# Kernel tuning notes

Measured on AMD Instinct MI355X. Metric: run time of the kernel, lower is better.

## Reference

```python
import jax, jax.numpy as jnp
import numpy as np

ROPE_BASE = 10000.0

def _rope_cos_sin(T, d, dtype):
    inv_freq = 1.0 / (ROPE_BASE ** (jnp.arange(0, d, 2, dtype=jnp.float32) / d))
    t = jnp.arange(T, dtype=jnp.float32)
    freqs = t[:, None] * inv_freq[None, :]           # [T, d/2]
    emb = jnp.concatenate([freqs, freqs], axis=-1)   # [T, d]
    return jnp.cos(emb).astype(dtype), jnp.sin(emb).astype(dtype)

def _rotate_half(x):
    x1, x2 = jnp.split(x, 2, axis=-1)
    return jnp.concatenate([-x2, x1], axis=-1)

def setup_inputs() -> dict:
    key = jax.random.key(0)
    k1, k2, k3, k4 = jax.random.split(key, 4)
    B, T, C, H = 4, 4096, 1024, 64
    x = jax.random.normal(k1, (B, T, C), dtype=jnp.float32)
    s = 1.0 / np.sqrt(C)
    Wq = jax.random.normal(k2, (H, C), dtype=jnp.float32) * s
    Wk = jax.random.normal(k3, (H, C), dtype=jnp.float32) * s
    Wv = jax.random.normal(k4, (H, C), dtype=jnp.float32) * s
    return {"x": x, "Wq": Wq, "Wk": Wk, "Wv": Wv}

def reference(x, Wq, Wk, Wv):
    B, T, C = x.shape
    H = Wq.shape[0]
    q = jnp.einsum('btc,hc->bth', x, Wq)
    k = jnp.einsum('btc,hc->bth', x, Wk)
    v = jnp.einsum('btc,hc->bth', x, Wv)
    cos, sin = _rope_cos_sin(T, H, x.dtype)
    q = q * cos + _rotate_half(q) * sin
    k = k * cos + _rotate_half(k) * sin
    # NOTE: original scales by dim_model**-0.5 (C), not head_size
    wei = jnp.einsum('bth,bsh->bts', q, k) * (C ** -0.5)
    causal = jnp.tril(jnp.ones((T, T), dtype=bool))
    wei = jnp.where(causal, wei, -jnp.inf)
    wei = jax.nn.softmax(wei, axis=-1)
    # dropout p=0.0 (identity)
    out = jnp.einsum('bts,bsh->bth', wei, v)
    return out
```

## Files before the change

kernel.cpp:

```cpp
#include <hip/hip_runtime.h>
#include <hip/hip_bf16.h>
#include <math.h>

typedef __attribute__((ext_vector_type(8))) __bf16 bf16x8;
typedef __attribute__((ext_vector_type(4))) float f32x4;
typedef __attribute__((ext_vector_type(16))) float f32x16;
typedef __attribute__((ext_vector_type(4))) float float4_t;
typedef __attribute__((ext_vector_type(4))) unsigned int uint4_t;

#define NB 4
#define TSEQ 4096
#define CD 1024
#define HD 64
#define NCH 8
#define CHT 8

static __device__ __forceinline__ unsigned short f2bf(float f) {
    union { float f; unsigned u; } v; v.f = f;
    unsigned r = v.u + 0x7fffu + ((v.u >> 16) & 1u);
    return (unsigned short)(r >> 16);
}
static __device__ __forceinline__ unsigned int pack2bf(float lo, float hi) {
    return (unsigned int)f2bf(lo) | ((unsigned int)f2bf(hi) << 16);
}

__global__ __launch_bounds__(256) void wcvt_kernel(const float* __restrict__ wq,
                                                   const float* __restrict__ wk,
                                                   const float* __restrict__ wv,
                                                   unsigned short* __restrict__ wb) {
    int i = blockIdx.x * 256 + threadIdx.x;
    int j = i >> 10;
    int col = i & 1023;
    int jb = j >> 4, off = j & 15;
    int sub = ((jb & 1) << 5) | ((jb & 2) << 3);
    int srcrow = (jb < 8) ? (sub + off) : ((jb - 8) * 16 + off);
    const float* src = (jb < 4) ? wq : ((jb < 8) ? wk : wv);
    wb[i] = f2bf(src[srcrow * 1024 + col]);
}

__global__ __launch_bounds__(256) void qkv_kernel(const float* __restrict__ x,
                                                  const unsigned short* __restrict__ wb,
                                                  unsigned short* __restrict__ qo,
                                                  unsigned short* __restrict__ ko,
                                                  unsigned short* __restrict__ vt) {
    __shared__ unsigned short xs[64][72];
    __shared__ unsigned short ws[64][72];
    const int tid = threadIdx.x;
    const int wave = tid >> 6, lane = tid & 63;
    const int lr = lane & 15;
    const int lk = (lane >> 4) << 3;
    const int rowg = (lane >> 4) << 2;
    const int row0 = blockIdx.x * 64;
    const int cb = blockIdx.y * 64;

    f32x4 acc[4];
#pragma unroll
    for (int i = 0; i < 4; ++i) acc[i] = (f32x4){0.f, 0.f, 0.f, 0.f};

    const int sr = tid >> 2;
    const int sc = (tid & 3) << 4;

    for (int k0 = 0; k0 < CD; k0 += 64) {
        __syncthreads();
        {
            const float4_t* s4 =
                reinterpret_cast<const float4_t*>(x + (size_t)(row0 + sr) * CD + k0 + sc);
            alignas(16) unsigned short tmp[16];
#pragma unroll
            for (int j = 0; j < 4; ++j) {
                float4_t f = s4[j];
#pragma unroll
                for (int e = 0; e < 4; ++e) tmp[j * 4 + e] = f2bf(f[e]);
            }
            *reinterpret_cast<uint4_t*>(&xs[sr][sc]) = *reinterpret_cast<const uint4_t*>(&tmp[0]);
            *reinterpret_cast<uint4_t*>(&xs[sr][sc + 8]) = *reinterpret_cast<const uint4_t*>(&tmp[8]);
        }
        {
            const uint4_t* wsrc =
                reinterpret_cast<const uint4_t*>(wb + (size_t)(cb + sr) * CD + k0 + sc);
            *reinterpret_cast<uint4_t*>(&ws[sr][sc]) = wsrc[0];
            *reinterpret_cast<uint4_t*>(&ws[sr][sc + 8]) = wsrc[1];
        }
        __syncthreads();
#pragma unroll
        for (int kk = 0; kk < 2; ++kk) {
            bf16x8 a = *reinterpret_cast<const bf16x8*>(&xs[wave * 16 + lr][kk * 32 + lk]);
#pragma unroll
            for (int c = 0; c < 4; ++c) {
                bf16x8 bfr = *reinterpret_cast<const bf16x8*>(&ws[c * 16 + lr][kk * 32 + lk]);
                acc[c] = __builtin_amdgcn_mfma_f32_16x16x32_bf16(a, bfr, acc[c], 0, 0, 0);
            }
        }
    }

    const int gr0 = row0 + wave * 16 + rowg;
    const int bidx = gr0 >> 12;
    const int tb = gr0 & (TSEQ - 1);
    if (blockIdx.y < 2) {
        unsigned short* o = (blockIdx.y == 0) ? qo : ko;
        const float sc2 = (blockIdx.y == 0) ? 0.045084218764560315f : 1.0f;
        const float l2b = 0.4152410118609215f;
        const float invf0 = exp2f(-(float)lr * l2b);
        const float invf1 = exp2f(-(float)(lr + 16) * l2b);
#pragma unroll
        for (int r = 0; r < 4; ++r) {
            float t = (float)(tb + r);
            float s0, c0, s1, c1;
            sincosf(t * invf0, &s0, &c0);
            sincosf(t * invf1, &s1, &c1);
            size_t ro = (size_t)(gr0 + r) * HD;
            float lo, hi;
            lo = acc[0][r]; hi = acc[1][r];
            o[ro + 0 + lr]  = f2bf((lo * c0 - hi * s0) * sc2);
            o[ro + 32 + lr] = f2bf((hi * c0 + lo * s0) * sc2);
            lo = acc[2][r]; hi = acc[3][r];
            o[ro + 16 + lr] = f2bf((lo * c1 - hi * s1) * sc2);
            o[ro + 48 + lr] = f2bf((hi * c1 + lo * s1) * sc2);
        }
    } else {
#pragma unroll
        for (int r = 0; r < 4; ++r) {
            size_t vbase = (size_t)bidx * HD * TSEQ + (size_t)(tb + r);
            vt[vbase + (size_t)(0 + lr) * TSEQ]  = f2bf(acc[0][r]);
            vt[vbase + (size_t)(16 + lr) * TSEQ] = f2bf(acc[1][r]);
            vt[vbase + (size_t)(32 + lr) * TSEQ] = f2bf(acc[2][r]);
            vt[vbase + (size_t)(48 + lr) * TSEQ] = f2bf(acc[3][r]);
        }
    }
}

__global__ __launch_bounds__(128, 3) void attn_partial(const unsigned short* __restrict__ q,
                                                       const unsigned short* __restrict__ k,
                                                       const unsigned short* __restrict__ vt,
                                                       float* __restrict__ po,
                                                       float* __restrict__ pm,
                                                       float* __restrict__ pl) {
    const int chunk = blockIdx.x, qt = blockIdx.y, b = blockIdx.z;
    const int kt0 = chunk * CHT;
    if (kt0 > qt) return;
    const int ktend = min(qt, kt0 + CHT - 1);

    __shared__ unsigned short ks[64][72];
    __shared__ unsigned short vs[64][72];
    const int tid = threadIdx.x;
    const int wave = tid >> 6, lane = tid & 63;
    const int l31 = lane & 31;
    const int h = lane >> 5;
    const int h8 = h << 3;
    const int qrow0 = qt * 64 + wave * 32;
    const int qpos = qrow0 + l31;

    const unsigned short* qb_ = q + ((size_t)(b * TSEQ + qpos)) * HD + h8;
    bf16x8 qf[4];
#pragma unroll
    for (int s = 0; s < 4; ++s)
        qf[s] = *reinterpret_cast<const bf16x8*>(qb_ + 16 * s);

    f32x16 oacc[2];
#pragma unroll
    for (int dt = 0; dt < 2; ++dt)
#pragma unroll
        for (int r = 0; r < 16; ++r) oacc[dt][r] = 0.f;
    float mreg = -INFINITY;
    float lsum = 0.f;

    const int srow = tid >> 1;
    const int scol = (tid & 1) << 5;
    const unsigned short* kbase = k + (size_t)b * TSEQ * HD;
    const unsigned short* vbase = vt + (size_t)b * HD * TSEQ;
    uint4_t kr[4], vr[4];
    {
        const int s0l = kt0 * 64;
        const unsigned short* kp = kbase + (size_t)(s0l + srow) * HD + scol;
        const unsigned short* vp = vbase + (size_t)srow * TSEQ + s0l + scol;
#pragma unroll
        for (int j = 0; j < 4; ++j) {
            kr[j] = *reinterpret_cast<const uint4_t*>(kp + 8 * j);
            vr[j] = *reinterpret_cast<const uint4_t*>(vp + 8 * j);
        }
    }

    for (int kt = kt0; kt <= ktend; ++kt) {
        const int s0 = kt * 64;
        __syncthreads();
#pragma unroll
        for (int j = 0; j < 4; ++j) {
            *reinterpret_cast<uint4_t*>(&ks[srow][scol + 8 * j]) = kr[j];
            *reinterpret_cast<uint4_t*>(&vs[srow][scol + 8 * j]) = vr[j];
        }
        __syncthreads();
        if (kt < ktend) {
            const int s0l = s0 + 64;
            const unsigned short* kp = kbase + (size_t)(s0l + srow) * HD + scol;
            const unsigned short* vp = vbase + (size_t)srow * TSEQ + s0l + scol;
#pragma unroll
            for (int j = 0; j < 4; ++j) {
                kr[j] = *reinterpret_cast<const uint4_t*>(kp + 8 * j);
                vr[j] = *reinterpret_cast<const uint4_t*>(vp + 8 * j);
            }
        }

        f32x16 sacc[2];
#pragma unroll
        for (int blk = 0; blk < 2; ++blk)
#pragma unroll
            for (int r = 0; r < 16; ++r) sacc[blk][r] = 0.f;
#pragma unroll
        for (int s = 0; s < 4; ++s) {
            bf16x8 ka = *reinterpret_cast<const bf16x8*>(&ks[l31][16 * s + h8]);
            bf16x8 kb2 = *reinterpret_cast<const bf16x8*>(&ks[32 + l31][16 * s + h8]);
            sacc[0] = __builtin_amdgcn_mfma_f32_32x32x16_bf16(ka, qf[s], sacc[0], 0, 0, 0);
            sacc[1] = __builtin_amdgcn_mfma_f32_32x32x16_bf16(kb2, qf[s], sacc[1], 0, 0, 0);
        }

        if (kt == qt) {
#pragma unroll
            for (int blk = 0; blk < 2; ++blk)
#pragma unroll
                for (int r = 0; r < 16; ++r) {
                    int kvpos = s0 + 32 * blk + (r & 3) + ((r >> 2) << 3) + (h << 2);
                    if (kvpos > qpos) sacc[blk][r] = -INFINITY;
                }
        }

        float mx = -INFINITY;
#pragma unroll
        for (int blk = 0; blk < 2; ++blk)
#pragma unroll
            for (int r = 0; r < 16; ++r) mx = fmaxf(mx, sacc[blk][r]);
        mx = fmaxf(mx, __shfl_xor(mx, 32, 64));
        float mnew = fmaxf(mreg, mx);
        float corr = __builtin_amdgcn_exp2f(mreg - mnew);
        mreg = mnew;
        float psum = 0.f;
        float pvv[2][16];
#pragma unroll
        for (int blk = 0; blk < 2; ++blk)
#pragma unroll
            for (int r = 0; r < 16; ++r) {
                float p = __builtin_amdgcn_exp2f(sacc[blk][r] - mnew);
                pvv[blk][r] = p;
                psum += p;
            }
        psum += __shfl_xor(psum, 32, 64);
        lsum = lsum * corr + psum;
#pragma unroll
        for (int dt = 0; dt < 2; ++dt)
#pragma unroll
            for (int r = 0; r < 16; ++r) oacc[dt][r] *= corr;

        unsigned int cw[2][4][2];
#pragma unroll
        for (int blk = 0; blk < 2; ++blk)
#pragma unroll
            for (int G = 0; G < 4; ++G) {
                cw[blk][G][0] = pack2bf(pvv[blk][4 * G], pvv[blk][4 * G + 1]);
                cw[blk][G][1] = pack2bf(pvv[blk][4 * G + 2], pvv[blk][4 * G + 3]);
            }

        const bool hif = (h == 1);
#pragma unroll
        for (int s = 0; s < 4; ++s) {
            const int blk = s >> 1, base = (s & 1) << 1;
            unsigned int a0 = cw[blk][base][0],     a1 = cw[blk][base][1];
            unsigned int b0 = cw[blk][base + 1][0], b1 = cw[blk][base + 1][1];
            unsigned int s0w = hif ? a0 : b0;
            unsigned int s1w = hif ? a1 : b1;
            unsigned int r0 = __shfl_xor(s0w, 32, 64);
            unsigned int r1 = __shfl_xor(s1w, 32, 64);
            uint4_t pw;
            pw[0] = hif ? r0 : a0;
            pw[1] = hif ? r1 : a1;
            pw[2] = hif ? b0 : r0;
            pw[3] = hif ? b1 : r1;
            bf16x8 pfrag = *reinterpret_cast<const bf16x8*>(&pw);
            bf16x8 v0 = *reinterpret_cast<const bf16x8*>(&vs[l31][16 * s + h8]);
            bf16x8 v1 = *reinterpret_cast<const bf16x8*>(&vs[32 + l31][16 * s + h8]);
            oacc[0] = __builtin_amdgcn_mfma_f32_32x32x16_bf16(v0, pfrag, oacc[0], 0, 0, 0);
            oacc[1] = __builtin_amdgcn_mfma_f32_32x32x16_bf16(v1, pfrag, oacc[1], 0, 0, 0);
        }
    }

    const int slot = (((b << 6) + qt) << 3) + chunk;
    float* pob = po + (size_t)slot * 4096;
#pragma unroll
    for (int dt = 0; dt < 2; ++dt)
#pragma unroll
        for (int r = 0; r < 16; ++r) {
            int d = 32 * dt + (r & 3) + ((r >> 2) << 3) + (h << 2);
            pob[d * 64 + wave * 32 + l31] = oacc[dt][r];
        }
    if (h == 0) {
        pm[slot * 64 + wave * 32 + l31] = mreg;
        pl[slot * 64 + wave * 32 + l31] = lsum;
    }
}

__global__ __launch_bounds__(256) void attn_combine(const float* __restrict__ po,
                                                    const float* __restrict__ pm,
                                                    const float* __restrict__ pl,
                                                    float* __restrict__ out) {
    __shared__ float sm[64][68];
    const int bq = blockIdx.x;
    const int qt = bq & 63;
    const int nch = (qt >> 3) + 1;
    const int qi = threadIdx.x & 63;
    const int dg = threadIdx.x >> 6;
    const int sbase = bq << 3;

    float M = -INFINITY;
    for (int c = 0; c < nch; ++c) M = fmaxf(M, pm[(sbase + c) * 64 + qi]);
    float L = 0.f;
    float acc[16];
#pragma unroll
    for (int j = 0; j < 16; ++j) acc[j] = 0.f;
    for (int c = 0; c < nch; ++c) {
        int s = sbase + c;
        float w = exp2f(pm[s * 64 + qi] - M);
        L += w * pl[s * 64 + qi];
        const float* p = po + (size_t)s * 4096 + qi;
#pragma unroll
        for (int j = 0; j < 16; ++j) acc[j] += w * p[(dg * 16 + j) * 64];
    }
    float inv = 1.f / L;
#pragma unroll
    for (int j = 0; j < 16; ++j) sm[qi][dg * 16 + j] = acc[j] * inv;
    __syncthreads();
    const int row = threadIdx.x >> 2;
    const int cg = (threadIdx.x & 3) << 4;
    float4_t* dst = reinterpret_cast<float4_t*>(out + (size_t)bq * 4096 + row * 64 + cg);
#pragma unroll
    for (int v4 = 0; v4 < 4; ++v4) {
        float4_t f;
#pragma unroll
        for (int e = 0; e < 4; ++e) f[e] = sm[row][cg + v4 * 4 + e];
        dst[v4] = f;
    }
}

extern "C" void kernel_launch(void* const* d_in, const int* in_sizes, int n_in,
                              void* d_out, int out_size, void* d_ws, size_t ws_size,
                              hipStream_t stream) {
    const float* x = (const float*)d_in[0];
    const float* wq = (const float*)d_in[1];
    const float* wk = (const float*)d_in[2];
    const float* wv = (const float*)d_in[3];
    float* out = (float*)d_out;

    unsigned short* wb = (unsigned short*)d_ws;
    unsigned short* qb = wb + 3 * HD * CD;
    unsigned short* kb = qb + (size_t)NB * TSEQ * HD;
    unsigned short* vtb = kb + (size_t)NB * TSEQ * HD;
    float* po = (float*)(vtb + (size_t)NB * TSEQ * HD);
    float* pm = po + (size_t)2048 * 4096;
    float* pl = pm + (size_t)2048 * 64;

    wcvt_kernel<<<768, 256, 0, stream>>>(wq, wk, wv, wb);
    qkv_kernel<<<dim3(256, 3), 256, 0, stream>>>(x, wb, qb, kb, vtb);
    attn_partial<<<dim3(NCH, 64, NB), 128, 0, stream>>>(qb, kb, vtb, po, pm, pl);
    attn_combine<<<NB * 64, 256, 0, stream>>>(po, pm, pl, out);
}
```

Measured before the change: 73.53 us.

## Double-buffer K/V tiles in attention, skip rescale when max unchanged, reorder QKV grid

The attention partial kernel now uses double-buffered shared memory for K/V tiles. The next tile is written into the alternate buffer during compute, which leaves one barrier per iteration instead of two. The online softmax uses tree reductions for the max and the sum, and skips the exp and output rescale when no lane sees a new max. The bf16 packing switches to native casts, and the QKV grid is flattened so the three column blocks of the same rows run adjacently, which should improve x reuse in cache. Occupancy hint drops from 3 to 2 blocks per CU to fit the doubled LDS and register pressure.

```diff
diff --git a/kernel.cpp b/kernel.cpp
--- a/kernel.cpp
+++ b/kernel.cpp
@@ -20,8 +20,10 @@
     unsigned r = v.u + 0x7fffu + ((v.u >> 16) & 1u);
     return (unsigned short)(r >> 16);
 }
-static __device__ __forceinline__ unsigned int pack2bf(float lo, float hi) {
-    return (unsigned int)f2bf(lo) | ((unsigned int)f2bf(hi) << 16);
+static __device__ __forceinline__ unsigned int pk2(float a, float b) {
+    union { __bf16 h[2]; unsigned int u; } x;
+    x.h[0] = (__bf16)a; x.h[1] = (__bf16)b;
+    return x.u;
 }
 
 __global__ __launch_bounds__(256) void wcvt_kernel(const float* __restrict__ wq,
@@ -50,8 +52,11 @@
     const int lr = lane & 15;
     const int lk = (lane >> 4) << 3;
     const int rowg = (lane >> 4) << 2;
-    const int row0 = blockIdx.x * 64;
-    const int cb = blockIdx.y * 64;
+    const int bid = blockIdx.x;
+    const int rb = bid / 3;
+    const int cbi = bid - rb * 3;
+    const int row0 = rb * 64;
+    const int cb = cbi * 64;
 
     f32x4 acc[4];
 #pragma unroll
@@ -96,9 +101,9 @@
     const int gr0 = row0 + wave * 16 + rowg;
     const int bidx = gr0 >> 12;
     const int tb = gr0 & (TSEQ - 1);
-    if (blockIdx.y < 2) {
-        unsigned short* o = (blockIdx.y == 0) ? qo : ko;
-        const float sc2 = (blockIdx.y == 0) ? 0.045084218764560315f : 1.0f;
+    if (cbi < 2) {
+        unsigned short* o = (cbi == 0) ? qo : ko;
+        const float sc2 = (cbi == 0) ? 0.045084218764560315f : 1.0f;
         const float l2b = 0.4152410118609215f;
         const float invf0 = exp2f(-(float)lr * l2b);
         const float invf1 = exp2f(-(float)(lr + 16) * l2b);
@@ -129,7 +134,7 @@
     }
 }
 
-__global__ __launch_bounds__(128, 3) void attn_partial(const unsigned short* __restrict__ q,
+__global__ __launch_bounds__(128, 2) void attn_partial(const unsigned short* __restrict__ q,
                                                        const unsigned short* __restrict__ k,
                                                        const unsigned short* __restrict__ vt,
                                                        float* __restrict__ po,
@@ -139,9 +144,10 @@
     const int kt0 = chunk * CHT;
     if (kt0 > qt) return;
     const int ktend = min(qt, kt0 + CHT - 1);
-
-    __shared__ unsigned short ks[64][72];
-    __shared__ unsigned short vs[64][72];
+    const int nt = ktend - kt0 + 1;
+
+    __shared__ unsigned short ks[2][64][72];
+    __shared__ unsigned short vs[2][64][72];
     const int tid = threadIdx.x;
     const int wave = tid >> 6, lane = tid & 63;
     const int l31 = lane & 31;
@@ -169,8 +175,9 @@
     const unsigned short* kbase = k + (size_t)b * TSEQ * HD;
     const unsigned short* vbase = vt + (size_t)b * HD * TSEQ;
     uint4_t kr[4], vr[4];
-    {
-        const int s0l = kt0 * 64;
+
+    auto loadtile = [&](int kt) {
+        const int s0l = kt * 64;
         const unsigned short* kp = kbase + (size_t)(s0l + srow) * HD + scol;
         const unsigned short* vp = vbase + (size_t)srow * TSEQ + s0l + scol;
 #pragma unroll
@@ -178,26 +185,27 @@
             kr[j] = *reinterpret_cast<const uint4_t*>(kp + 8 * j);
             vr[j] = *reinterpret_cast<const uint4_t*>(vp + 8 * j);
         }
-    }
-
-    for (int kt = kt0; kt <= ktend; ++kt) {
+    };
+    auto writetile = [&](int p) {
+#pragma unroll
+        for (int j = 0; j < 4; ++j) {
+            *reinterpret_cast<uint4_t*>(&ks[p][srow][scol + 8 * j]) = kr[j];
+            *reinterpret_cast<uint4_t*>(&vs[p][srow][scol + 8 * j]) = vr[j];
+        }
+    };
+
+    loadtile(kt0);
+    writetile(0);
+    if (nt > 1) loadtile(kt0 + 1);
+    __syncthreads();
+
+    for (int it = 0; it < nt; ++it) {
+        const int kt = kt0 + it;
         const int s0 = kt * 64;
-        __syncthreads();
-#pragma unroll
-        for (int j = 0; j < 4; ++j) {
-            *reinterpret_cast<uint4_t*>(&ks[srow][scol + 8 * j]) = kr[j];
-            *reinterpret_cast<uint4_t*>(&vs[srow][scol + 8 * j]) = vr[j];
-        }
-        __syncthreads();
-        if (kt < ktend) {
-            const int s0l = s0 + 64;
-            const unsigned short* kp = kbase + (size_t)(s0l + srow) * HD + scol;
-            const unsigned short* vp = vbase + (size_t)srow * TSEQ + s0l + scol;
-#pragma unroll
-            for (int j = 0; j < 4; ++j) {
-                kr[j] = *reinterpret_cast<const uint4_t*>(kp + 8 * j);
-                vr[j] = *reinterpret_cast<const uint4_t*>(vp + 8 * j);
-            }
+        const int p = it & 1;
+        if (it + 1 < nt) {
+            writetile(p ^ 1);
+            if (it + 2 < nt) loadtile(kt + 2);
         }
 
         f32x16 sacc[2];
@@ -207,8 +215,8 @@
             for (int r = 0; r < 16; ++r) sacc[blk][r] = 0.f;
 #pragma unroll
         for (int s = 0; s < 4; ++s) {
-            bf16x8 ka = *reinterpret_cast<const bf16x8*>(&ks[l31][16 * s + h8]);
-            bf16x8 kb2 = *reinterpret_cast<const bf16x8*>(&ks[32 + l31][16 * s + h8]);
+            bf16x8 ka = *reinterpret_cast<const bf16x8*>(&ks[p][l31][16 * s + h8]);
+            bf16x8 kb2 = *reinterpret_cast<const bf16x8*>(&ks[p][32 + l31][16 * s + h8]);
             sacc[0] = __builtin_amdgcn_mfma_f32_32x32x16_bf16(ka, qf[s], sacc[0], 0, 0, 0);
             sacc[1] = __builtin_amdgcn_mfma_f32_32x32x16_bf16(kb2, qf[s], sacc[1], 0, 0, 0);
         }
@@ -223,39 +231,56 @@
                 }
         }
 
-        float mx = -INFINITY;
+        float tm[8];
+#pragma unroll
+        for (int r = 0; r < 8; ++r)
+            tm[r] = fmaxf(fmaxf(sacc[0][r], sacc[0][r + 8]),
+                          fmaxf(sacc[1][r], sacc[1][r + 8]));
+#pragma unroll
+        for (int r = 0; r < 4; ++r) tm[r] = fmaxf(tm[r], tm[r + 4]);
+        float mx = fmaxf(fmaxf(tm[0], tm[1]), fmaxf(tm[2], tm[3]));
+        mx = fmaxf(mx, __shfl_xor(mx, 32, 64));
+
+        const bool newmax = !__all(mx <= mreg);
+        float mnew = mreg, corr = 1.f;
+        if (newmax) {
+            mnew = fmaxf(mreg, mx);
+            corr = __builtin_amdgcn_exp2f(mreg - mnew);
+            mreg = mnew;
+        }
+
+        float pvv[2][16];
 #pragma unroll
         for (int blk = 0; blk < 2; ++blk)
 #pragma unroll
-            for (int r = 0; r < 16; ++r) mx = fmaxf(mx, sacc[blk][r]);
-        mx = fmaxf(mx, __shfl_xor(mx, 32, 64));
-        float mnew = fmaxf(mreg, mx);
-        float corr = __builtin_amdgcn_exp2f(mreg - mnew);
-        mreg = mnew;
-        float psum = 0.f;
-        float pvv[2][16];
+            for (int r = 0; r < 16; ++r)
+                pvv[blk][r] = __builtin_amdgcn_exp2f(sacc[blk][r] - mnew);
+        float ts[8];
+#pragma unroll
+        for (int r = 0; r < 8; ++r)
+            ts[r] = (pvv[0][r] + pvv[0][r + 8]) + (pvv[1][r] + pvv[1][r + 8]);
+#pragma unroll
+        for (int r = 0; r < 4; ++r) ts[r] += ts[r + 4];
+        float psum = (ts[0] + ts[1]) + (ts[2] + ts[3]);
+        psum += __shfl_xor(psum, 32, 64);
+
+        if (newmax) {
+            lsum = lsum * corr + psum;
+#pragma unroll
+            for (int dt = 0; dt < 2; ++dt)
+#pragma unroll
+                for (int r = 0; r < 16; ++r) oacc[dt][r] *= corr;
+        } else {
+            lsum += psum;
+        }
+
+        unsigned int cw[2][4][2];
 #pragma unroll
         for (int blk = 0; blk < 2; ++blk)
 #pragma unroll
-            for (int r = 0; r < 16; ++r) {
-                float p = __builtin_amdgcn_exp2f(sacc[blk][r] - mnew);
-                pvv[blk][r] = p;
-                psum += p;
-            }
-        psum += __shfl_xor(psum, 32, 64);
-        lsum = lsum * corr + psum;
-#pragma unroll
-        for (int dt = 0; dt < 2; ++dt)
-#pragma unroll
-            for (int r = 0; r < 16; ++r) oacc[dt][r] *= corr;
-
-        unsigned int cw[2][4][2];
-#pragma unroll
-        for (int blk = 0; blk < 2; ++blk)
-#pragma unroll
             for (int G = 0; G < 4; ++G) {
-                cw[blk][G][0] = pack2bf(pvv[blk][4 * G], pvv[blk][4 * G + 1]);
-                cw[blk][G][1] = pack2bf(pvv[blk][4 * G + 2], pvv[blk][4 * G + 3]);
+                cw[blk][G][0] = pk2(pvv[blk][4 * G], pvv[blk][4 * G + 1]);
+                cw[blk][G][1] = pk2(pvv[blk][4 * G + 2], pvv[blk][4 * G + 3]);
             }
 
         const bool hif = (h == 1);
@@ -274,11 +299,12 @@
             pw[2] = hif ? b0 : r0;
             pw[3] = hif ? b1 : r1;
             bf16x8 pfrag = *reinterpret_cast<const bf16x8*>(&pw);
-            bf16x8 v0 = *reinterpret_cast<const bf16x8*>(&vs[l31][16 * s + h8]);
-            bf16x8 v1 = *reinterpret_cast<const bf16x8*>(&vs[32 + l31][16 * s + h8]);
+            bf16x8 v0 = *reinterpret_cast<const bf16x8*>(&vs[p][l31][16 * s + h8]);
+            bf16x8 v1 = *reinterpret_cast<const bf16x8*>(&vs[p][32 + l31][16 * s + h8]);
             oacc[0] = __builtin_amdgcn_mfma_f32_32x32x16_bf16(v0, pfrag, oacc[0], 0, 0, 0);
             oacc[1] = __builtin_amdgcn_mfma_f32_32x32x16_bf16(v1, pfrag, oacc[1], 0, 0, 0);
         }
+        __syncthreads();
     }
 
     const int slot = (((b << 6) + qt) << 3) + chunk;
@@ -356,7 +382,7 @@
     float* pl = pm + (size_t)2048 * 64;
 
     wcvt_kernel<<<768, 256, 0, stream>>>(wq, wk, wv, wb);
-    qkv_kernel<<<dim3(256, 3), 256, 0, stream>>>(x, wb, qb, kb, vtb);
+    qkv_kernel<<<768, 256, 0, stream>>>(x, wb, qb, kb, vtb);
     attn_partial<<<dim3(NCH, 64, NB), 128, 0, stream>>>(qb, kb, vtb, po, pm, pl);
     attn_combine<<<NB * 64, 256, 0, stream>>>(po, pm, pl, out);
 }
```

Measured after the change: 86.96 us. +18.3%, slower.

## Halve split-K chunk size, store partial outputs as bf16, use native bf16 packing

Applied to the files above, without the earlier changes.

The number of key chunks per query tile goes from 8 to 16, with each chunk covering 4 key tiles instead of 8. This gives more parallel blocks and a shorter critical path on the causal attention. Partial outputs are now written as bf16 instead of fp32, which halves the partial-buffer traffic that the larger split would otherwise double. The combine kernel now reads bf16 partials over up to twice as many chunks. Probability packing uses the compiler's native bf16 conversion in place of the manual rounding. The bf16 partials lose precision, and combine does more work per query tile.

```diff
diff --git a/kernel.cpp b/kernel.cpp
--- a/kernel.cpp
+++ b/kernel.cpp
@@ -12,16 +12,22 @@
 #define TSEQ 4096
 #define CD 1024
 #define HD 64
-#define NCH 8
-#define CHT 8
+#define NCH 16
+#define CHT 4
 
 static __device__ __forceinline__ unsigned short f2bf(float f) {
     union { float f; unsigned u; } v; v.f = f;
     unsigned r = v.u + 0x7fffu + ((v.u >> 16) & 1u);
     return (unsigned short)(r >> 16);
 }
-static __device__ __forceinline__ unsigned int pack2bf(float lo, float hi) {
-    return (unsigned int)f2bf(lo) | ((unsigned int)f2bf(hi) << 16);
+static __device__ __forceinline__ float bf2f(unsigned short u) {
+    union { unsigned int i; float f; } v; v.i = ((unsigned int)u) << 16;
+    return v.f;
+}
+static __device__ __forceinline__ unsigned int pk2(float a, float b) {
+    union { __bf16 h[2]; unsigned int u; } x;
+    x.h[0] = (__bf16)a; x.h[1] = (__bf16)b;
+    return x.u;
 }
 
 __global__ __launch_bounds__(256) void wcvt_kernel(const float* __restrict__ wq,
@@ -51,7 +57,8 @@
     const int lk = (lane >> 4) << 3;
     const int rowg = (lane >> 4) << 2;
     const int row0 = blockIdx.x * 64;
-    const int cb = blockIdx.y * 64;
+    const int cbi = blockIdx.y;
+    const int cb = cbi * 64;
 
     f32x4 acc[4];
 #pragma unroll
@@ -96,9 +103,9 @@
     const int gr0 = row0 + wave * 16 + rowg;
     const int bidx = gr0 >> 12;
     const int tb = gr0 & (TSEQ - 1);
-    if (blockIdx.y < 2) {
-        unsigned short* o = (blockIdx.y == 0) ? qo : ko;
-        const float sc2 = (blockIdx.y == 0) ? 0.045084218764560315f : 1.0f;
+    if (cbi < 2) {
+        unsigned short* o = (cbi == 0) ? qo : ko;
+        const float sc2 = (cbi == 0) ? 0.045084218764560315f : 1.0f;
         const float l2b = 0.4152410118609215f;
         const float invf0 = exp2f(-(float)lr * l2b);
         const float invf1 = exp2f(-(float)(lr + 16) * l2b);
@@ -132,7 +139,7 @@
 __global__ __launch_bounds__(128, 3) void attn_partial(const unsigned short* __restrict__ q,
                                                        const unsigned short* __restrict__ k,
                                                        const unsigned short* __restrict__ vt,
-                                                       float* __restrict__ po,
+                                                       unsigned short* __restrict__ po,
                                                        float* __restrict__ pm,
                                                        float* __restrict__ pl) {
     const int chunk = blockIdx.x, qt = blockIdx.y, b = blockIdx.z;
@@ -254,8 +261,8 @@
         for (int blk = 0; blk < 2; ++blk)
 #pragma unroll
             for (int G = 0; G < 4; ++G) {
-                cw[blk][G][0] = pack2bf(pvv[blk][4 * G], pvv[blk][4 * G + 1]);
-                cw[blk][G][1] = pack2bf(pvv[blk][4 * G + 2], pvv[blk][4 * G + 3]);
+                cw[blk][G][0] = pk2(pvv[blk][4 * G], pvv[blk][4 * G + 1]);
+                cw[blk][G][1] = pk2(pvv[blk][4 * G + 2], pvv[blk][4 * G + 3]);
             }
 
         const bool hif = (h == 1);
@@ -281,14 +288,14 @@
         }
     }
 
-    const int slot = (((b << 6) + qt) << 3) + chunk;
-    float* pob = po + (size_t)slot * 4096;
+    const int slot = (((b << 6) + qt) << 4) + chunk;
+    unsigned short* pob = po + (size_t)slot * 4096;
 #pragma unroll
     for (int dt = 0; dt < 2; ++dt)
 #pragma unroll
         for (int r = 0; r < 16; ++r) {
             int d = 32 * dt + (r & 3) + ((r >> 2) << 3) + (h << 2);
-            pob[d * 64 + wave * 32 + l31] = oacc[dt][r];
+            pob[d * 64 + wave * 32 + l31] = f2bf(oacc[dt][r]);
         }
     if (h == 0) {
         pm[slot * 64 + wave * 32 + l31] = mreg;
@@ -296,17 +303,17 @@
     }
 }
 
-__global__ __launch_bounds__(256) void attn_combine(const float* __restrict__ po,
+__global__ __launch_bounds__(256) void attn_combine(const unsigned short* __restrict__ po,
                                                     const float* __restrict__ pm,
                                                     const float* __restrict__ pl,
                                                     float* __restrict__ out) {
     __shared__ float sm[64][68];
     const int bq = blockIdx.x;
     const int qt = bq & 63;
-    const int nch = (qt >> 3) + 1;
+    const int nch = (qt >> 2) + 1;
     const int qi = threadIdx.x & 63;
     const int dg = threadIdx.x >> 6;
-    const int sbase = bq << 3;
+    const int sbase = bq << 4;
 
     float M = -INFINITY;
     for (int c = 0; c < nch; ++c) M = fmaxf(M, pm[(sbase + c) * 64 + qi]);
@@ -318,9 +325,9 @@
         int s = sbase + c;
         float w = exp2f(pm[s * 64 + qi] - M);
         L += w * pl[s * 64 + qi];
-        const float* p = po + (size_t)s * 4096 + qi;
-#pragma unroll
-        for (int j = 0; j < 16; ++j) acc[j] += w * p[(dg * 16 + j) * 64];
+        const unsigned short* p = po + (size_t)s * 4096 + qi;
+#pragma unroll
+        for (int j = 0; j < 16; ++j) acc[j] += w * bf2f(p[(dg * 16 + j) * 64]);
     }
     float inv = 1.f / L;
 #pragma unroll
@@ -351,12 +358,12 @@
     unsigned short* qb = wb + 3 * HD * CD;
     unsigned short* kb = qb + (size_t)NB * TSEQ * HD;
     unsigned short* vtb = kb + (size_t)NB * TSEQ * HD;
-    float* po = (float*)(vtb + (size_t)NB * TSEQ * HD);
-    float* pm = po + (size_t)2048 * 4096;
-    float* pl = pm + (size_t)2048 * 64;
+    unsigned short* pob = vtb + (size_t)NB * TSEQ * HD;
+    float* pm = (float*)(pob + (size_t)4096 * 4096);
+    float* pl = pm + (size_t)4096 * 64;
 
     wcvt_kernel<<<768, 256, 0, stream>>>(wq, wk, wv, wb);
     qkv_kernel<<<dim3(256, 3), 256, 0, stream>>>(x, wb, qb, kb, vtb);
-    attn_partial<<<dim3(NCH, 64, NB), 128, 0, stream>>>(qb, kb, vtb, po, pm, pl);
-    attn_combine<<<NB * 64, 256, 0, stream>>>(po, pm, pl, out);
-}
+    attn_partial<<<dim3(NCH, 64, NB), 128, 0, stream>>>(qb, kb, vtb, pob, pm, pl);
+    attn_combine<<<NB * 64, 256, 0, stream>>>(pob, pm, pl, out);
+}
```

Result: no change. 73.31 us (-0.3%).
